# Performance work log

Measured on AMD Instinct MI355X. Metric: run time of the kernel, lower is better.

## Reference

```python
import jax, jax.numpy as jnp
import numpy as np

B, C, H, W = 4, 64, 128, 128
O = 64
K, S, P, D = 3, 1, 1, 1
K2 = K * K
Ho = (H + 2 * P - D * (K - 1) - 1) // S + 1
Wo = (W + 2 * P - D * (K - 1) - 1) // S + 1


def setup_inputs() -> dict:
    key = jax.random.key(0)
    k1, k2, k3, k4, k5 = jax.random.split(key, 5)
    x = jax.random.normal(k1, (B, C, H, W), dtype=jnp.float32)
    fan = C * K2
    # offset conv: out_channels = 2*n_offsets*K*K = 18; small init so offsets are ~O(1) px
    offset_w = jax.random.normal(k2, (2 * K2, C, K, K), dtype=jnp.float32) * (0.1 / np.sqrt(fan))
    offset_b = jax.random.normal(k3, (2 * K2,), dtype=jnp.float32) * 0.01
    deform_w = jax.random.normal(k4, (O, C, K, K), dtype=jnp.float32) * (1.0 / np.sqrt(fan))
    deform_b = jax.random.normal(k5, (O,), dtype=jnp.float32) * 0.01
    return {"x": x, "offset_w": offset_w, "offset_b": offset_b,
            "deform_w": deform_w, "deform_b": deform_b}


def _conv2d(x, w, b):
    y = jax.lax.conv_general_dilated(
        x, w, window_strides=(S, S), padding=[(P, P), (P, P)],
        rhs_dilation=(D, D), dimension_numbers=("NCHW", "OIHW", "NCHW"))
    return y + b[None, :, None, None]


def _gather(flat, iy, ix, h, w):
    # flat: [B, C, H*W]; iy/ix: [B, K2, Ho, Wo] int32
    valid = (iy >= 0) & (iy < h) & (ix >= 0) & (ix < w)
    idx = jnp.clip(iy, 0, h - 1) * w + jnp.clip(ix, 0, w - 1)
    b = flat.shape[0]
    v = jax.vmap(lambda f, i: f[:, i])(flat, idx.reshape(b, -1))  # [B, C, K2*Ho*Wo]
    v = v.reshape(b, flat.shape[1], *idx.shape[1:])               # [B, C, K2, Ho, Wo]
    return v * valid[:, None].astype(flat.dtype)


def _deform_conv(x, offset, w, b):
    # offset: [B, 2*K2, Ho, Wo] laid out as (dy, dx) pairs per kernel tap (torchvision order)
    off = offset.reshape(B, K2, 2, Ho, Wo)
    dy, dx = off[:, :, 0], off[:, :, 1]                           # [B, K2, Ho, Wo]
    ky = (jnp.arange(K2) // K * D).astype(jnp.float32)
    kx = (jnp.arange(K2) % K * D).astype(jnp.float32)
    base_y = (jnp.arange(Ho) * S - P).astype(jnp.float32)
    base_x = (jnp.arange(Wo) * S - P).astype(jnp.float32)
    py = dy + base_y[None, None, :, None] + ky[None, :, None, None]
    px = dx + base_x[None, None, None, :] + kx[None, :, None, None]

    y0 = jnp.floor(py); x0 = jnp.floor(px)
    wy = py - y0; wx = px - x0
    y0i = y0.astype(jnp.int32); x0i = x0.astype(jnp.int32)
    flat = x.reshape(B, C, H * W)
    w00 = ((1 - wy) * (1 - wx))[:, None]
    w01 = ((1 - wy) * wx)[:, None]
    w10 = (wy * (1 - wx))[:, None]
    w11 = (wy * wx)[:, None]
    sampled = (_gather(flat, y0i, x0i, H, W) * w00
               + _gather(flat, y0i, x0i + 1, H, W) * w01
               + _gather(flat, y0i + 1, x0i, H, W) * w10
               + _gather(flat, y0i + 1, x0i + 1, H, W) * w11)  # [B, C, K2, Ho, Wo]
    out = jnp.einsum("bckhw,ock->bohw", sampled, w.reshape(O, C, K2))
    return out + b[None, :, None, None]


def reference(x, offset_w, offset_b, deform_w, deform_b):
    offset = _conv2d(x, offset_w, offset_b)
    return _deform_conv(x, offset, deform_w, deform_b)
```

## Files before the change

### kernel.cpp

```cpp
#include <hip/hip_runtime.h>

#define BB 4
#define CC 64
#define HH 128
#define WW 128
#define OO 64
#define HWs (HH*WW)
#define R9 9
#define XW 37

typedef _Float16 f16;
typedef _Float16 f16x8 __attribute__((ext_vector_type(8)));
typedef _Float16 f16x2 __attribute__((ext_vector_type(2)));
typedef float f32x4 __attribute__((ext_vector_type(4)));

__device__ __forceinline__ size_t xt_idx(int b, int y, int x) {
    return (((size_t)b * HH + y) * WW + x) * CC;
}

__global__ __launch_bounds__(256) void prep_all(const float* __restrict__ x,
                                                const float* __restrict__ offw,
                                                const float* __restrict__ dw,
                                                f16* __restrict__ xt,
                                                f16* __restrict__ wA_off,
                                                f16* __restrict__ wA_def) {
    const int bid = blockIdx.x;
    const int tid = threadIdx.x;
    if (bid < 512) {
        const int b = bid >> 7, y = bid & 127;
        const int px = tid & 127, half = tid >> 7;
        const float* src = x + (size_t)b * CC * HWs + (size_t)half * 32 * HWs + y * WW + px;
        f16* dst = xt + xt_idx(b, y, px) + half * 32;
        #pragma unroll
        for (int cg = 0; cg < 4; ++cg) {
            f16x8 v;
            #pragma unroll
            for (int j = 0; j < 8; ++j)
                v[j] = (f16)src[(size_t)(cg * 8 + j) * HWs];
            *(f16x8*)(dst + cg * 8) = v;
        }
    } else {
        const int t = (bid - 512) * 256 + tid;
        const int l = t & 63;
        const int idx = t >> 6;
        f16x8 v;
        if (idx < 36) {
            const int mt = idx & 1, ks = idx >> 1;
            const int o = mt * 16 + (l & 15);
            const int tap = ks >> 1, ky = tap / 3, kx = tap % 3;
            #pragma unroll
            for (int i = 0; i < 8; ++i) {
                const int c = (ks & 1) * 32 + (l >> 4) * 8 + i;
                v[i] = (o < 18) ? (f16)offw[((o * CC + c) * 3 + ky) * 3 + kx] : (f16)0.f;
            }
            *(f16x8*)(wA_off + (size_t)(idx * 64 + l) * 8) = v;
        } else if (idx < 108) {
            const int id2 = idx - 36;
            const int mt = id2 & 3, ks = (id2 >> 2) & 1, tap = id2 >> 3;
            const int o = mt * 16 + (l & 15);
            #pragma unroll
            for (int i = 0; i < 8; ++i) {
                const int c = ks * 32 + (l >> 4) * 8 + i;
                v[i] = (f16)dw[(size_t)(o * CC + c) * 9 + tap];
            }
            *(f16x8*)(wA_def + (size_t)(id2 * 64 + l) * 8) = v;
        }
    }
}

__device__ __forceinline__ f16x8 combine4(f16x8 p00, f16x8 p01, f16x8 p10, f16x8 p11,
                                          f16 h00, f16 h01, f16 h10, f16 h11) {
    const f16x8 W00 = {h00,h00,h00,h00,h00,h00,h00,h00};
    const f16x8 W01 = {h01,h01,h01,h01,h01,h01,h01,h01};
    const f16x8 W10 = {h10,h10,h10,h10,h10,h10,h10,h10};
    const f16x8 W11 = {h11,h11,h11,h11,h11,h11,h11,h11};
    return p00 * W00 + p01 * W01 + p10 * W10 + p11 * W11;
}

__global__ __launch_bounds__(512) void deform_mfma(
    const f16* __restrict__ xt,
    const f16* __restrict__ wA_off,
    const float* __restrict__ offb,
    const f16* __restrict__ wA_def,
    const float* __restrict__ dbias,
    float* __restrict__ out)
{
    extern __shared__ __align__(16) char lds[];
    char*  wdef_l = lds;
    char*  woff_l = lds + 73728;
    char*  winp   = lds + 110592;
    float* offs   = (float*)(lds + 153216);

    const int tid = threadIdx.x;
    const int bid0 = blockIdx.x;
    const int bid = (bid0 & 7) * 64 + (bid0 >> 3);
    const int b  = bid >> 7;
    const int rg = (bid >> 2) & 31;
    const int pg = bid & 3;
    const int r0 = rg * 4, px0 = pg * 32;

    const int wid = tid >> 6, l = tid & 63;
    const int ri = wid >> 1, pt = wid & 1;
    const int pxs = l & 15, cg = l >> 4;
    const int pxl = pt * 16 + pxs;
    const int row = r0 + ri;
    const int gpx = px0 + pxl;
    const int slot = ri * 32 + pxl;

    #pragma unroll
    for (int it = 0; it < 9; ++it) {
        const int i = tid + it * 512;
        *(f16x8*)(wdef_l + i * 16) = *(const f16x8*)((const char*)wA_def + (size_t)i * 16);
    }
    #pragma unroll
    for (int it = 0; it < 5; ++it) {
        const int i = tid + it * 512;
        if (i < 2304)
            *(f16x8*)(woff_l + i * 16) = *(const f16x8*)((const char*)wA_off + (size_t)i * 16);
    }
    #pragma unroll
    for (int it = 0; it < 6; ++it) {
        const int i = tid + it * 512;
        if (i < R9 * XW * 8) {
            const int s = i / (XW * 8), rem = i - s * (XW * 8);
            const int xw = rem >> 3, ch8 = rem & 7;
            const int gy = r0 - 2 + s, gx = px0 - 2 + xw;
            f16x8 v = {};
            if (gy >= 0 && gy < HH && gx >= 0 && gx < WW)
                v = *(const f16x8*)(xt + xt_idx(b, gy, gx) + ch8 * 8);
            *(f16x8*)(winp + ((s * XW + xw) * 8 + (ch8 ^ ((xw + s) & 7))) * 16) = v;
        }
    }
    __syncthreads();

    {
        f32x4 oa0 = {0,0,0,0}, oa1 = {0,0,0,0};
        #pragma unroll
        for (int ks = 0; ks < 18; ++ks) {
            const int tap = ks >> 1, chalf = ks & 1;
            const int ky = tap / 3, kx = tap - ky * 3;
            const int s = ri + 1 + ky;
            const int xw = pxl + 1 + kx;
            const int ch8 = chalf * 4 + cg;
            const f16x8 bf = *(const f16x8*)(winp + ((s * XW + xw) * 8 + (ch8 ^ ((xw + s) & 7))) * 16);
            const f16x8 a0 = *(const f16x8*)(woff_l + ((ks * 2 + 0) * 64 + l) * 16);
            const f16x8 a1 = *(const f16x8*)(woff_l + ((ks * 2 + 1) * 64 + l) * 16);
            oa0 = __builtin_amdgcn_mfma_f32_16x16x32_f16(a0, bf, oa0, 0, 0, 0);
            oa1 = __builtin_amdgcn_mfma_f32_16x16x32_f16(a1, bf, oa1, 0, 0, 0);
        }
        #pragma unroll
        for (int reg = 0; reg < 4; ++reg) {
            const int c0 = cg * 4 + reg;
            offs[c0 * 128 + slot] = oa0[reg] + offb[c0];
            const int c1 = c0 + 16;
            if (c1 < 18) offs[c1 * 128 + slot] = oa1[reg] + offb[c1];
        }
    }
    __syncthreads();

    int o00[9], o01[9], o10[9], o11[9];
    f16x2 hA[9], hB[9];
    unsigned okm = 0;
    #pragma unroll
    for (int t = 0; t < 9; ++t) {
        const int ky = t / 3, kx = t - ky * 3;
        const float dy = offs[(2 * t) * 128 + slot], dx = offs[(2 * t + 1) * 128 + slot];
        const float py  = (float)(row - 1 + ky) + dy;
        const float pxf = (float)(gpx - 1 + kx) + dx;
        const float y0f = floorf(py), x0f = floorf(pxf);
        const float wy = py - y0f, wx = pxf - x0f;
        const int y0 = (int)y0f, x0 = (int)x0f;
        const int y1 = y0 + 1, x1 = x0 + 1;
        const bool vy0 = (y0 >= 0) & (y0 < HH), vy1 = (y1 >= 0) & (y1 < HH);
        const bool vx0 = (x0 >= 0) & (x0 < WW), vx1 = (x1 >= 0) & (x1 < WW);
        hA[t][0] = (f16)((1.f - wy) * (1.f - wx) * (float)(vy0 & vx0));
        hA[t][1] = (f16)((1.f - wy) * wx         * (float)(vy0 & vx1));
        hB[t][0] = (f16)(wy * (1.f - wx)         * (float)(vy1 & vx0));
        hB[t][1] = (f16)(wy * wx                 * (float)(vy1 & vx1));
        const int cy0 = min(max(y0, 0), HH - 1), cy1 = min(max(y1, 0), HH - 1);
        const int cx0 = min(max(x0, 0), WW - 1), cx1 = min(max(x1, 0), WW - 1);
        const int s0 = cy0 - (r0 - 2), s1 = cy1 - (r0 - 2);
        const int u0 = cx0 - (px0 - 2), u1 = cx1 - (px0 - 2);
        const int ok = (s0 >= 0) & (s0 < R9) & (s1 >= 0) & (s1 < R9) &
                       (u0 >= 0) & (u0 < XW) & (u1 >= 0) & (u1 < XW);
        if (__all(ok)) okm |= (1u << t);
        const int s0c = min(max(s0, 0), R9 - 1), s1c = min(max(s1, 0), R9 - 1);
        const int u0c = min(max(u0, 0), XW - 1), u1c = min(max(u1, 0), XW - 1);
        o00[t] = ((s0c * XW + u0c) * 8 + (cg ^ ((u0c + s0c) & 7))) * 16;
        o01[t] = ((s0c * XW + u1c) * 8 + (cg ^ ((u1c + s0c) & 7))) * 16;
        o10[t] = ((s1c * XW + u0c) * 8 + (cg ^ ((u0c + s1c) & 7))) * 16;
        o11[t] = ((s1c * XW + u1c) * 8 + (cg ^ ((u1c + s1c) & 7))) * 16;
    }

    f32x4 acc0 = {0,0,0,0}, acc1 = {0,0,0,0}, acc2 = {0,0,0,0}, acc3 = {0,0,0,0};

    if (okm == 0x1FFu) {
        #pragma unroll
        for (int j = 0; j < 18; ++j) {
            const int t = j >> 1, fl = (j & 1) << 6;
            const f16x8 p00 = *(const f16x8*)(winp + (o00[t] ^ fl));
            const f16x8 p01 = *(const f16x8*)(winp + (o01[t] ^ fl));
            const f16x8 p10 = *(const f16x8*)(winp + (o10[t] ^ fl));
            const f16x8 p11 = *(const f16x8*)(winp + (o11[t] ^ fl));
            const f16x8 bf = combine4(p00, p01, p10, p11,
                                      hA[t][0], hA[t][1], hB[t][0], hB[t][1]);
            const char* wa = wdef_l + ((j * 4) * 64 + l) * 16;
            acc0 = __builtin_amdgcn_mfma_f32_16x16x32_f16(*(const f16x8*)(wa + 0 * 1024), bf, acc0, 0, 0, 0);
            acc1 = __builtin_amdgcn_mfma_f32_16x16x32_f16(*(const f16x8*)(wa + 1 * 1024), bf, acc1, 0, 0, 0);
            acc2 = __builtin_amdgcn_mfma_f32_16x16x32_f16(*(const f16x8*)(wa + 2 * 1024), bf, acc2, 0, 0, 0);
            acc3 = __builtin_amdgcn_mfma_f32_16x16x32_f16(*(const f16x8*)(wa + 3 * 1024), bf, acc3, 0, 0, 0);
        }
    } else {
        #pragma unroll
        for (int t = 0; t < 9; ++t) {
            #pragma unroll
            for (int cpass = 0; cpass < 2; ++cpass) {
                const int flip = cpass << 6;
                f16x8 bf;
                if ((okm >> t) & 1) {
                    const f16x8 p00 = *(const f16x8*)(winp + (o00[t] ^ flip));
                    const f16x8 p01 = *(const f16x8*)(winp + (o01[t] ^ flip));
                    const f16x8 p10 = *(const f16x8*)(winp + (o10[t] ^ flip));
                    const f16x8 p11 = *(const f16x8*)(winp + (o11[t] ^ flip));
                    bf = combine4(p00, p01, p10, p11,
                                  hA[t][0], hA[t][1], hB[t][0], hB[t][1]);
                } else {
                    const int ky = t / 3, kx = t - ky * 3;
                    const float dy = offs[(2 * t) * 128 + slot], dx = offs[(2 * t + 1) * 128 + slot];
                    const float py  = (float)(row - 1 + ky) + dy;
                    const float pxf = (float)(gpx - 1 + kx) + dx;
                    const int y0 = (int)floorf(py), x0 = (int)floorf(pxf);
                    const int cy0 = min(max(y0, 0), HH - 1), cy1 = min(max(y0 + 1, 0), HH - 1);
                    const int cx0 = min(max(x0, 0), WW - 1), cx1 = min(max(x0 + 1, 0), WW - 1);
                    const int ch8 = cpass * 4 + cg;
                    const f16x8 p00 = *(const f16x8*)(xt + xt_idx(b, cy0, cx0) + ch8 * 8);
                    const f16x8 p01 = *(const f16x8*)(xt + xt_idx(b, cy0, cx1) + ch8 * 8);
                    const f16x8 p10 = *(const f16x8*)(xt + xt_idx(b, cy1, cx0) + ch8 * 8);
                    const f16x8 p11 = *(const f16x8*)(xt + xt_idx(b, cy1, cx1) + ch8 * 8);
                    bf = combine4(p00, p01, p10, p11,
                                  hA[t][0], hA[t][1], hB[t][0], hB[t][1]);
                }
                const char* wa = wdef_l + (((t * 2 + cpass) * 4) * 64 + l) * 16;
                acc0 = __builtin_amdgcn_mfma_f32_16x16x32_f16(*(const f16x8*)(wa + 0 * 1024), bf, acc0, 0, 0, 0);
                acc1 = __builtin_amdgcn_mfma_f32_16x16x32_f16(*(const f16x8*)(wa + 1 * 1024), bf, acc1, 0, 0, 0);
                acc2 = __builtin_amdgcn_mfma_f32_16x16x32_f16(*(const f16x8*)(wa + 2 * 1024), bf, acc2, 0, 0, 0);
                acc3 = __builtin_amdgcn_mfma_f32_16x16x32_f16(*(const f16x8*)(wa + 3 * 1024), bf, acc3, 0, 0, 0);
            }
        }
    }

    #pragma unroll
    for (int mt = 0; mt < 4; ++mt) {
        const f32x4 a = (mt == 0) ? acc0 : (mt == 1) ? acc1 : (mt == 2) ? acc2 : acc3;
        #pragma unroll
        for (int reg = 0; reg < 4; ++reg) {
            const int o = mt * 16 + cg * 4 + reg;
            out[(((size_t)b * OO + o) * HH + row) * WW + gpx] = a[reg] + dbias[o];
        }
    }
}

extern "C" void kernel_launch(void* const* d_in, const int* in_sizes, int n_in,
                              void* d_out, int out_size, void* d_ws, size_t ws_size,
                              hipStream_t stream) {
    const float* x     = (const float*)d_in[0];
    const float* offw  = (const float*)d_in[1];
    const float* offb  = (const float*)d_in[2];
    const float* dw    = (const float*)d_in[3];
    const float* dbias = (const float*)d_in[4];
    float* out = (float*)d_out;

    const size_t XT_BYTES    = (size_t)BB * HH * WW * CC * sizeof(f16);
    const size_t WAOFF_BYTES = 36 * 64 * 8 * sizeof(f16);

    f16* xt     = (f16*)d_ws;
    f16* wa_off = (f16*)((char*)d_ws + XT_BYTES);
    f16* wa_def = (f16*)((char*)d_ws + XT_BYTES + WAOFF_BYTES);
    (void)ws_size; (void)in_sizes; (void)n_in; (void)out_size;

    const int LDS_BYTES = 162432;
    (void)hipFuncSetAttribute((const void*)deform_mfma,
                              hipFuncAttributeMaxDynamicSharedMemorySize, LDS_BYTES);

    prep_all<<<512 + 27, 256, 0, stream>>>(x, offw, dw, xt, wa_off, wa_def);
    deform_mfma<<<512, 512, LDS_BYTES, stream>>>(xt, wa_off, offb, wa_def, dbias, out);
}
```

Measured before the change: 39.40 us.

## Shrink deform tile, read weights from global, drop big LDS for occupancy

The per-block tile is halved from 4x32 to 4x16 pixels, giving 1024 blocks of 256 threads. The deform and offset-conv weight matrices are no longer staged into LDS; MFMA A-operands are loaded straight from global/L2. LDS use falls from about 160 KB to about 28 KB, so several blocks can share a CU, with launch bounds raised to target that. The cost is repeated weight fetches through the cache per block and a larger halo overhead relative to the smaller tile.

```diff
diff --git a/kernel.cpp b/kernel.cpp
--- a/kernel.cpp
+++ b/kernel.cpp
@@ -7,7 +7,7 @@
 #define OO 64
 #define HWs (HH*WW)
 #define R9 9
-#define XW 37
+#define XW 20
 
 typedef _Float16 f16;
 typedef _Float16 f16x8 __attribute__((ext_vector_type(8)));
@@ -77,7 +77,7 @@
     return p00 * W00 + p01 * W01 + p10 * W10 + p11 * W11;
 }
 
-__global__ __launch_bounds__(512) void deform_mfma(
+__global__ __launch_bounds__(256, 5) void deform_mfma(
     const f16* __restrict__ xt,
     const f16* __restrict__ wA_off,
     const float* __restrict__ offb,
@@ -85,42 +85,26 @@
     const float* __restrict__ dbias,
     float* __restrict__ out)
 {
-    extern __shared__ __align__(16) char lds[];
-    char*  wdef_l = lds;
-    char*  woff_l = lds + 73728;
-    char*  winp   = lds + 110592;
-    float* offs   = (float*)(lds + 153216);
+    __shared__ __align__(16) char win[R9 * XW * 8 * 16];
+    __shared__ float offs[18][64];
 
     const int tid = threadIdx.x;
     const int bid0 = blockIdx.x;
-    const int bid = (bid0 & 7) * 64 + (bid0 >> 3);
-    const int b  = bid >> 7;
-    const int rg = (bid >> 2) & 31;
-    const int pg = bid & 3;
-    const int r0 = rg * 4, px0 = pg * 32;
-
-    const int wid = tid >> 6, l = tid & 63;
-    const int ri = wid >> 1, pt = wid & 1;
+    const int bid = (bid0 & 7) * 128 + (bid0 >> 3);
+    const int b  = bid >> 8;
+    const int rg = (bid >> 3) & 31;
+    const int pg = bid & 7;
+    const int r0 = rg * 4, px0 = pg * 16;
+
+    const int ri = tid >> 6, l = tid & 63;
     const int pxs = l & 15, cg = l >> 4;
-    const int pxl = pt * 16 + pxs;
     const int row = r0 + ri;
-    const int gpx = px0 + pxl;
-    const int slot = ri * 32 + pxl;
-
-    #pragma unroll
-    for (int it = 0; it < 9; ++it) {
-        const int i = tid + it * 512;
-        *(f16x8*)(wdef_l + i * 16) = *(const f16x8*)((const char*)wA_def + (size_t)i * 16);
-    }
-    #pragma unroll
-    for (int it = 0; it < 5; ++it) {
-        const int i = tid + it * 512;
-        if (i < 2304)
-            *(f16x8*)(woff_l + i * 16) = *(const f16x8*)((const char*)wA_off + (size_t)i * 16);
-    }
+    const int gpx = px0 + pxs;
+    const int slot = ri * 16 + pxs;
+
     #pragma unroll
     for (int it = 0; it < 6; ++it) {
-        const int i = tid + it * 512;
+        const int i = tid + it * 256;
         if (i < R9 * XW * 8) {
             const int s = i / (XW * 8), rem = i - s * (XW * 8);
             const int xw = rem >> 3, ch8 = rem & 7;
@@ -128,7 +112,7 @@
             f16x8 v = {};
             if (gy >= 0 && gy < HH && gx >= 0 && gx < WW)
                 v = *(const f16x8*)(xt + xt_idx(b, gy, gx) + ch8 * 8);
-            *(f16x8*)(winp + ((s * XW + xw) * 8 + (ch8 ^ ((xw + s) & 7))) * 16) = v;
+            *(f16x8*)(win + ((s * XW + xw) * 8 + (ch8 ^ ((xw + s) & 7))) * 16) = v;
         }
     }
     __syncthreads();
@@ -140,20 +124,20 @@
             const int tap = ks >> 1, chalf = ks & 1;
             const int ky = tap / 3, kx = tap - ky * 3;
             const int s = ri + 1 + ky;
-            const int xw = pxl + 1 + kx;
+            const int xw = pxs + 1 + kx;
             const int ch8 = chalf * 4 + cg;
-            const f16x8 bf = *(const f16x8*)(winp + ((s * XW + xw) * 8 + (ch8 ^ ((xw + s) & 7))) * 16);
-            const f16x8 a0 = *(const f16x8*)(woff_l + ((ks * 2 + 0) * 64 + l) * 16);
-            const f16x8 a1 = *(const f16x8*)(woff_l + ((ks * 2 + 1) * 64 + l) * 16);
+            const f16x8 bf = *(const f16x8*)(win + ((s * XW + xw) * 8 + (ch8 ^ ((xw + s) & 7))) * 16);
+            const f16x8 a0 = *(const f16x8*)(wA_off + (size_t)((ks * 2 + 0) * 64 + l) * 8);
+            const f16x8 a1 = *(const f16x8*)(wA_off + (size_t)((ks * 2 + 1) * 64 + l) * 8);
             oa0 = __builtin_amdgcn_mfma_f32_16x16x32_f16(a0, bf, oa0, 0, 0, 0);
             oa1 = __builtin_amdgcn_mfma_f32_16x16x32_f16(a1, bf, oa1, 0, 0, 0);
         }
         #pragma unroll
         for (int reg = 0; reg < 4; ++reg) {
             const int c0 = cg * 4 + reg;
-            offs[c0 * 128 + slot] = oa0[reg] + offb[c0];
+            offs[c0][slot] = oa0[reg] + offb[c0];
             const int c1 = c0 + 16;
-            if (c1 < 18) offs[c1 * 128 + slot] = oa1[reg] + offb[c1];
+            if (c1 < 18) offs[c1][slot] = oa1[reg] + offb[c1];
         }
     }
     __syncthreads();
@@ -164,7 +148,7 @@
     #pragma unroll
     for (int t = 0; t < 9; ++t) {
         const int ky = t / 3, kx = t - ky * 3;
-        const float dy = offs[(2 * t) * 128 + slot], dx = offs[(2 * t + 1) * 128 + slot];
+        const float dy = offs[2 * t][slot], dx = offs[2 * t + 1][slot];
         const float py  = (float)(row - 1 + ky) + dy;
         const float pxf = (float)(gpx - 1 + kx) + dx;
         const float y0f = floorf(py), x0f = floorf(pxf);
@@ -193,22 +177,23 @@
     }
 
     f32x4 acc0 = {0,0,0,0}, acc1 = {0,0,0,0}, acc2 = {0,0,0,0}, acc3 = {0,0,0,0};
+    const f16* wbase = wA_def + (size_t)l * 8;
 
     if (okm == 0x1FFu) {
         #pragma unroll
         for (int j = 0; j < 18; ++j) {
             const int t = j >> 1, fl = (j & 1) << 6;
-            const f16x8 p00 = *(const f16x8*)(winp + (o00[t] ^ fl));
-            const f16x8 p01 = *(const f16x8*)(winp + (o01[t] ^ fl));
-            const f16x8 p10 = *(const f16x8*)(winp + (o10[t] ^ fl));
-            const f16x8 p11 = *(const f16x8*)(winp + (o11[t] ^ fl));
+            const f16x8 p00 = *(const f16x8*)(win + (o00[t] ^ fl));
+            const f16x8 p01 = *(const f16x8*)(win + (o01[t] ^ fl));
+            const f16x8 p10 = *(const f16x8*)(win + (o10[t] ^ fl));
+            const f16x8 p11 = *(const f16x8*)(win + (o11[t] ^ fl));
             const f16x8 bf = combine4(p00, p01, p10, p11,
                                       hA[t][0], hA[t][1], hB[t][0], hB[t][1]);
-            const char* wa = wdef_l + ((j * 4) * 64 + l) * 16;
-            acc0 = __builtin_amdgcn_mfma_f32_16x16x32_f16(*(const f16x8*)(wa + 0 * 1024), bf, acc0, 0, 0, 0);
-            acc1 = __builtin_amdgcn_mfma_f32_16x16x32_f16(*(const f16x8*)(wa + 1 * 1024), bf, acc1, 0, 0, 0);
-            acc2 = __builtin_amdgcn_mfma_f32_16x16x32_f16(*(const f16x8*)(wa + 2 * 1024), bf, acc2, 0, 0, 0);
-            acc3 = __builtin_amdgcn_mfma_f32_16x16x32_f16(*(const f16x8*)(wa + 3 * 1024), bf, acc3, 0, 0, 0);
+            const f16* wa = wbase + (size_t)j * 2048;
+            acc0 = __builtin_amdgcn_mfma_f32_16x16x32_f16(*(const f16x8*)(wa + 0 * 512), bf, acc0, 0, 0, 0);
+            acc1 = __builtin_amdgcn_mfma_f32_16x16x32_f16(*(const f16x8*)(wa + 1 * 512), bf, acc1, 0, 0, 0);
+            acc2 = __builtin_amdgcn_mfma_f32_16x16x32_f16(*(const f16x8*)(wa + 2 * 512), bf, acc2, 0, 0, 0);
+            acc3 = __builtin_amdgcn_mfma_f32_16x16x32_f16(*(const f16x8*)(wa + 3 * 512), bf, acc3, 0, 0, 0);
         }
     } else {
         #pragma unroll
@@ -218,15 +203,15 @@
                 const int flip = cpass << 6;
                 f16x8 bf;
                 if ((okm >> t) & 1) {
-                    const f16x8 p00 = *(const f16x8*)(winp + (o00[t] ^ flip));
-                    const f16x8 p01 = *(const f16x8*)(winp + (o01[t] ^ flip));
-                    const f16x8 p10 = *(const f16x8*)(winp + (o10[t] ^ flip));
-                    const f16x8 p11 = *(const f16x8*)(winp + (o11[t] ^ flip));
+                    const f16x8 p00 = *(const f16x8*)(win + (o00[t] ^ flip));
+                    const f16x8 p01 = *(const f16x8*)(win + (o01[t] ^ flip));
+                    const f16x8 p10 = *(const f16x8*)(win + (o10[t] ^ flip));
+                    const f16x8 p11 = *(const f16x8*)(win + (o11[t] ^ flip));
                     bf = combine4(p00, p01, p10, p11,
                                   hA[t][0], hA[t][1], hB[t][0], hB[t][1]);
                 } else {
                     const int ky = t / 3, kx = t - ky * 3;
-                    const float dy = offs[(2 * t) * 128 + slot], dx = offs[(2 * t + 1) * 128 + slot];
+                    const float dy = offs[2 * t][slot], dx = offs[2 * t + 1][slot];
                     const float py  = (float)(row - 1 + ky) + dy;
                     const float pxf = (float)(gpx - 1 + kx) + dx;
                     const int y0 = (int)floorf(py), x0 = (int)floorf(pxf);
@@ -240,11 +225,11 @@
                     bf = combine4(p00, p01, p10, p11,
                                   hA[t][0], hA[t][1], hB[t][0], hB[t][1]);
                 }
-                const char* wa = wdef_l + (((t * 2 + cpass) * 4) * 64 + l) * 16;
-                acc0 = __builtin_amdgcn_mfma_f32_16x16x32_f16(*(const f16x8*)(wa + 0 * 1024), bf, acc0, 0, 0, 0);
-                acc1 = __builtin_amdgcn_mfma_f32_16x16x32_f16(*(const f16x8*)(wa + 1 * 1024), bf, acc1, 0, 0, 0);
-                acc2 = __builtin_amdgcn_mfma_f32_16x16x32_f16(*(const f16x8*)(wa + 2 * 1024), bf, acc2, 0, 0, 0);
-                acc3 = __builtin_amdgcn_mfma_f32_16x16x32_f16(*(const f16x8*)(wa + 3 * 1024), bf, acc3, 0, 0, 0);
+                const f16* wa = wbase + (size_t)(t * 2 + cpass) * 2048;
+                acc0 = __builtin_amdgcn_mfma_f32_16x16x32_f16(*(const f16x8*)(wa + 0 * 512), bf, acc0, 0, 0, 0);
+                acc1 = __builtin_amdgcn_mfma_f32_16x16x32_f16(*(const f16x8*)(wa + 1 * 512), bf, acc1, 0, 0, 0);
+                acc2 = __builtin_amdgcn_mfma_f32_16x16x32_f16(*(const f16x8*)(wa + 2 * 512), bf, acc2, 0, 0, 0);
+                acc3 = __builtin_amdgcn_mfma_f32_16x16x32_f16(*(const f16x8*)(wa + 3 * 512), bf, acc3, 0, 0, 0);
             }
         }
     }
@@ -278,10 +263,6 @@
     f16* wa_def = (f16*)((char*)d_ws + XT_BYTES + WAOFF_BYTES);
     (void)ws_size; (void)in_sizes; (void)n_in; (void)out_size;
 
-    const int LDS_BYTES = 162432;
-    (void)hipFuncSetAttribute((const void*)deform_mfma,
-                              hipFuncAttributeMaxDynamicSharedMemorySize, LDS_BYTES);
-
     prep_all<<<512 + 27, 256, 0, stream>>>(x, offw, dw, xt, wa_off, wa_def);
-    deform_mfma<<<512, 512, LDS_BYTES, stream>>>(xt, wa_off, offb, wa_def, dbias, out);
-}
+    deform_mfma<<<1024, 256, 0, stream>>>(xt, wa_off, offb, wa_def, dbias, out);
+}
```

Result: no change. 39.88 us (+1.2%).
